# Optimization experiments

Hardware: AMD Instinct MI355X
Metric: run time of the kernel (lower is better)

## Reference

```python
import jax, jax.numpy as jnp
import numpy as np

A = 0.2  # margin (init kwarg a)


def setup_inputs() -> dict:
    key = jax.random.key(0)
    k1, k2, k3, k4 = jax.random.split(key, 4)
    B, D, N_IDS = 160, 128, 64
    anchor = jax.random.normal(k1, (B, D), dtype=jnp.float32)
    positive = jax.random.normal(k2, (B, D), dtype=jnp.float32)
    negative = jax.random.normal(k3, (B, D), dtype=jnp.float32)
    ind = jax.random.randint(k4, (3 * B, 1), 0, N_IDS, dtype=jnp.int32)
    return {"anchor": anchor, "positive": positive, "negative": negative, "ind": ind}


def reference(anchor, positive, negative, ind):
    # embeddings: [N, D], N = 3*B
    emb = jnp.concatenate([anchor, positive, negative], axis=0)
    labels = ind[:, 0]  # [N]
    gram = emb @ emb.T                     # [N, N]
    sq = jnp.diagonal(gram)                # squared norms, [N]
    # squared euclidean pairwise distances, clamped at 0
    pd = jnp.maximum(sq[None, :] + sq[:, None] - 2.0 * gram, 0.0)
    same = labels[:, None] == labels[None, :]   # [N, N]
    # triplet_diff[i, j, k] = pd[i, j] - pd[j, k] + a   (broadcast [N,N,1] - [1,N,N])
    td = pd[:, :, None] - pd[None, :, :] + A    # [N, N, N]
    # zero where labels[i] != labels[j]  (triplet_diff[label_diff] = 0)
    # zero where labels[j] == labels[k]  (triplet_diff[:, label_same] = 0)
    keep = same[:, :, None] & (~same)[None, :, :]
    # torch.diag(torch.zeros(N, long)) is an NxN zero long tensor; advanced
    # indexing with it sets triplet_diff[0, :, :] = 0 — reproduce faithfully.
    keep = keep.at[0].set(False)
    hard = keep & (td > 0)
    cnt = jnp.sum(hard).astype(td.dtype)
    s = jnp.sum(jnp.where(hard, td, 0.0))
    # mean over hard (positive, unmasked) triplets; 0 if none exist
    return jnp.where(cnt > 0, s / jnp.maximum(cnt, 1.0), jnp.zeros((), td.dtype))
```

## Files before the change

### kernel.cpp

```cpp
#include <hip/hip_runtime.h>


#define NROWS 480
#define DDIM  128
#define BLK   256
#define MARGIN 0.2f

__device__ __forceinline__ const float* emb_row(const float* a, const float* p,
                                                const float* n, int r) {
  if (r < 160) return a + r * DDIM;
  if (r < 320) return p + (r - 160) * DDIM;
  return n + (r - 320) * DDIM;
}

__global__ __launch_bounds__(BLK) void triplet_rows(
    const float* __restrict__ anch, const float* __restrict__ posi,
    const float* __restrict__ nega, const int* __restrict__ ind,
    float* __restrict__ partials) {
  __shared__ float ei[DDIM];
  __shared__ float pdrow[NROWS];
  __shared__ int   labels[NROWS];
  __shared__ int   poslist[NROWS];
  __shared__ int   npos;
  __shared__ float red_s[BLK / 64], red_c[BLK / 64];

  const int tid = threadIdx.x;
  const int a = blockIdx.x;

  for (int t = tid; t < NROWS; t += BLK) labels[t] = ind[t];
  if (tid == 0) npos = 0;
  {
    const float* ra = emb_row(anch, posi, nega, a);
    if (tid < DDIM) ei[tid] = ra[tid];
  }
  __syncthreads();

  const int la = labels[a];
  for (int r = tid; r < NROWS; r += BLK) {
    const float4* er = (const float4*)emb_row(anch, posi, nega, r);
    float d2 = 0.f;
#pragma unroll
    for (int dd = 0; dd < DDIM / 4; ++dd) {
      float4 b = er[dd];
      float x0 = ei[4 * dd + 0] - b.x;
      float x1 = ei[4 * dd + 1] - b.y;
      float x2 = ei[4 * dd + 2] - b.z;
      float x3 = ei[4 * dd + 3] - b.w;
      d2 += x0 * x0 + x1 * x1 + x2 * x2 + x3 * x3;
    }
    pdrow[r] = d2;
    if (labels[r] == la && r != 0) {
      int slot = atomicAdd(&npos, 1);
      poslist[slot] = r;
    }
  }
  __syncthreads();

  float s = 0.f, c = 0.f;
  {
    const int k0 = tid, k1 = tid + BLK;
    const float pk0 = pdrow[k0];
    const bool g0 = (labels[k0] != la);
    float pk1 = 0.f;
    bool g1 = false;
    if (k1 < NROWS) { pk1 = pdrow[k1]; g1 = (labels[k1] != la); }
    const int np = npos;
    for (int ii = 0; ii < np; ++ii) {
      const float tb = pdrow[poslist[ii]] + MARGIN;
      float td0 = tb - pk0;
      if (g0 && td0 > 0.f) { s += td0; c += 1.f; }
      float td1 = tb - pk1;
      if (g1 && td1 > 0.f) { s += td1; c += 1.f; }
    }
  }

  for (int off = 32; off > 0; off >>= 1) {
    s += __shfl_down(s, off, 64);
    c += __shfl_down(c, off, 64);
  }
  const int wave = tid >> 6, lane = tid & 63;
  if (lane == 0) { red_s[wave] = s; red_c[wave] = c; }
  __syncthreads();
  if (tid == 0) {
    float ts = 0.f, tc = 0.f;
    for (int w = 0; w < BLK / 64; ++w) { ts += red_s[w]; tc += red_c[w]; }
    partials[2 * a] = ts;
    partials[2 * a + 1] = tc;
  }
}

__global__ void triplet_finalize(const float* __restrict__ partials,
                                 float* __restrict__ out) {
  const int t = threadIdx.x;
  double s = 0.0, c = 0.0;
  for (int b = t; b < NROWS; b += 64) {
    s += (double)partials[2 * b];
    c += (double)partials[2 * b + 1];
  }
  for (int off = 32; off > 0; off >>= 1) {
    s += __shfl_down(s, off, 64);
    c += __shfl_down(c, off, 64);
  }
  if (t == 0) out[0] = (c > 0.0) ? (float)(s / c) : 0.0f;
}

extern "C" void kernel_launch(void* const* d_in, const int* in_sizes, int n_in,
                              void* d_out, int out_size, void* d_ws, size_t ws_size,
                              hipStream_t stream) {
  const float* anch = (const float*)d_in[0];
  const float* posi = (const float*)d_in[1];
  const float* nega = (const float*)d_in[2];
  const int*   ind  = (const int*)d_in[3];
  float* out = (float*)d_out;
  float* partials = (float*)d_ws;

  triplet_rows<<<NROWS, BLK, 0, stream>>>(anch, posi, nega, ind, partials);
  triplet_finalize<<<1, 64, 0, stream>>>(partials, out);
}
```

Baseline: 77.84 us.

## Fuse row partials and final reduction via cooperative grid sync

Replaces the two-kernel sequence (per-anchor partials, then a single-block finalize) with one cooperative kernel. Every block computes its partial, a grid-wide sync follows, and block 0 then reduces all partials in double precision. The aim is to remove the second kernel launch and its inter-kernel gap. In exchange it adds a grid barrier across 480 blocks and the overhead of a cooperative launch, and it falls back to the two-kernel path if the cooperative launch fails.

New measurement: 133.7 us. 1.72x slower.

```diff
diff --git a/kernel.cpp b/kernel.cpp
--- a/kernel.cpp
+++ b/kernel.cpp
@@ -1,5 +1,8 @@
 #include <hip/hip_runtime.h>
+#include <hip/hip_cooperative_groups.h>
 
+
+namespace cg = cooperative_groups;
 
 #define NROWS 480
 #define DDIM  128
@@ -13,22 +16,16 @@
   return n + (r - 320) * DDIM;
 }
 
-__global__ __launch_bounds__(BLK) void triplet_rows(
+__device__ __forceinline__ void anchor_partial(
     const float* __restrict__ anch, const float* __restrict__ posi,
     const float* __restrict__ nega, const int* __restrict__ ind,
-    float* __restrict__ partials) {
-  __shared__ float ei[DDIM];
-  __shared__ float pdrow[NROWS];
-  __shared__ int   labels[NROWS];
-  __shared__ int   poslist[NROWS];
-  __shared__ int   npos;
-  __shared__ float red_s[BLK / 64], red_c[BLK / 64];
-
+    float* __restrict__ partials, float* ei, float* pdrow, int* labels,
+    int* poslist, int* npos, float* red_s, float* red_c) {
   const int tid = threadIdx.x;
   const int a = blockIdx.x;
 
   for (int t = tid; t < NROWS; t += BLK) labels[t] = ind[t];
-  if (tid == 0) npos = 0;
+  if (tid == 0) *npos = 0;
   {
     const float* ra = emb_row(anch, posi, nega, a);
     if (tid < DDIM) ei[tid] = ra[tid];
@@ -50,7 +47,7 @@
     }
     pdrow[r] = d2;
     if (labels[r] == la && r != 0) {
-      int slot = atomicAdd(&npos, 1);
+      int slot = atomicAdd(npos, 1);
       poslist[slot] = r;
     }
   }
@@ -64,7 +61,7 @@
     float pk1 = 0.f;
     bool g1 = false;
     if (k1 < NROWS) { pk1 = pdrow[k1]; g1 = (labels[k1] != la); }
-    const int np = npos;
+    const int np = *npos;
     for (int ii = 0; ii < np; ++ii) {
       const float tb = pdrow[poslist[ii]] + MARGIN;
       float td0 = tb - pk0;
@@ -89,6 +86,20 @@
   }
 }
 
+__global__ __launch_bounds__(BLK) void triplet_rows(
+    const float* __restrict__ anch, const float* __restrict__ posi,
+    const float* __restrict__ nega, const int* __restrict__ ind,
+    float* __restrict__ partials) {
+  __shared__ float ei[DDIM];
+  __shared__ float pdrow[NROWS];
+  __shared__ int   labels[NROWS];
+  __shared__ int   poslist[NROWS];
+  __shared__ int   npos;
+  __shared__ float red_s[BLK / 64], red_c[BLK / 64];
+  anchor_partial(anch, posi, nega, ind, partials, ei, pdrow, labels, poslist,
+                 &npos, red_s, red_c);
+}
+
 __global__ void triplet_finalize(const float* __restrict__ partials,
                                  float* __restrict__ out) {
   const int t = threadIdx.x;
@@ -104,6 +115,46 @@
   if (t == 0) out[0] = (c > 0.0) ? (float)(s / c) : 0.0f;
 }
 
+__global__ __launch_bounds__(BLK) void triplet_coop(
+    const float* __restrict__ anch, const float* __restrict__ posi,
+    const float* __restrict__ nega, const int* __restrict__ ind,
+    float* __restrict__ partials, float* __restrict__ out) {
+  __shared__ float ei[DDIM];
+  __shared__ float pdrow[NROWS];
+  __shared__ int   labels[NROWS];
+  __shared__ int   poslist[NROWS];
+  __shared__ int   npos;
+  __shared__ float red_s[BLK / 64], red_c[BLK / 64];
+  __shared__ double dred_s[BLK / 64], dred_c[BLK / 64];
+
+  anchor_partial(anch, posi, nega, ind, partials, ei, pdrow, labels, poslist,
+                 &npos, red_s, red_c);
+  if (threadIdx.x == 0) __threadfence();
+
+  cg::this_grid().sync();
+
+  if (blockIdx.x == 0) {
+    const int tid = threadIdx.x;
+    double ds = 0.0, dc = 0.0;
+    for (int b = tid; b < NROWS; b += BLK) {
+      ds += (double)partials[2 * b];
+      dc += (double)partials[2 * b + 1];
+    }
+    for (int off = 32; off > 0; off >>= 1) {
+      ds += __shfl_down(ds, off, 64);
+      dc += __shfl_down(dc, off, 64);
+    }
+    const int wave = tid >> 6, lane = tid & 63;
+    if (lane == 0) { dred_s[wave] = ds; dred_c[wave] = dc; }
+    __syncthreads();
+    if (tid == 0) {
+      double ts = 0.0, tc = 0.0;
+      for (int w = 0; w < BLK / 64; ++w) { ts += dred_s[w]; tc += dred_c[w]; }
+      out[0] = (tc > 0.0) ? (float)(ts / tc) : 0.0f;
+    }
+  }
+}
+
 extern "C" void kernel_launch(void* const* d_in, const int* in_sizes, int n_in,
                               void* d_out, int out_size, void* d_ws, size_t ws_size,
                               hipStream_t stream) {
@@ -114,6 +165,12 @@
   float* out = (float*)d_out;
   float* partials = (float*)d_ws;
 
-  triplet_rows<<<NROWS, BLK, 0, stream>>>(anch, posi, nega, ind, partials);
-  triplet_finalize<<<1, 64, 0, stream>>>(partials, out);
+  void* args[] = {(void*)&anch, (void*)&posi, (void*)&nega, (void*)&ind,
+                  (void*)&partials, (void*)&out};
+  hipError_t err = hipLaunchCooperativeKernel(
+      (void*)triplet_coop, dim3(NROWS), dim3(BLK), args, 0, stream);
+  if (err != hipSuccess) {
+    triplet_rows<<<NROWS, BLK, 0, stream>>>(anch, posi, nega, ind, partials);
+    triplet_finalize<<<1, 64, 0, stream>>>(partials, out);
+  }
 }
```
